# Kernel tuning notes

Hardware: AMD Instinct MI355X
Metric: run time of the kernel (lower is better)

## Reference

```python
import jax, jax.numpy as jnp
import numpy as np

NEG_SLOPE = 0.2
EPS = 1e-16  # PyG softmax denominator epsilon


def _gatv2_layer(x, src, dst, n_nodes, W_l, W_r, att, bias):
    """Single-head GATv2Conv (PyG defaults, self loops already in src/dst).
    x: [N, F_in]; src/dst: [E]; W_l/W_r: [F_in, F_out]; att: [F_out]; bias: [F_out].
    """
    x_l = x @ W_l                       # source transform [N, F_out]
    x_r = x @ W_r                       # target transform [N, F_out]
    # per-edge attention logit: a^T LeakyReLU(x_l[j] + x_r[i])
    e = jax.nn.leaky_relu(x_l[src] + x_r[dst], NEG_SLOPE) @ att  # [E]
    # softmax over incoming edges of each destination node
    e_max = jax.ops.segment_max(e, dst, num_segments=n_nodes)    # [N]
    ex = jnp.exp(e - e_max[dst])                                  # [E]
    denom = jax.ops.segment_sum(ex, dst, num_segments=n_nodes)   # [N]
    alpha = ex / (denom[dst] + EPS)                               # [E]
    out = jax.ops.segment_sum(alpha[:, None] * x_l[src], dst, num_segments=n_nodes)
    return out + bias


def setup_inputs() -> dict:
    key = jax.random.key(0)
    N, E = 50000, 800000
    IN, HID, OUT = 128, 64, 64
    ks = jax.random.split(key, 12)
    x = jax.random.normal(ks[0], (N, IN), dtype=jnp.float32)
    edge_index = jax.random.randint(ks[1], (2, E), 0, N, dtype=jnp.int64)
    s1 = float(1.0 / np.sqrt(IN))
    s2 = float(1.0 / np.sqrt(HID))
    return {
        "x": x,
        "edge_index": edge_index,
        "W1_l": jax.random.uniform(ks[2], (IN, HID), jnp.float32, -s1, s1),
        "W1_r": jax.random.uniform(ks[3], (IN, HID), jnp.float32, -s1, s1),
        "att1": jax.random.uniform(ks[4], (HID,), jnp.float32, -s2, s2),
        "b1": jnp.zeros((HID,), jnp.float32),
        "W2_l": jax.random.uniform(ks[5], (HID, OUT), jnp.float32, -s2, s2),
        "W2_r": jax.random.uniform(ks[6], (HID, OUT), jnp.float32, -s2, s2),
        "att2": jax.random.uniform(ks[7], (OUT,), jnp.float32, -s2, s2),
        "b2": jnp.zeros((OUT,), jnp.float32),
    }


def reference(x, edge_index, W1_l, W1_r, att1, b1, W2_l, W2_r, att2, b2):
    n = x.shape[0]
    loop = jnp.arange(n, dtype=edge_index.dtype)
    src = jnp.concatenate([edge_index[0], loop])  # add self loops (PyG default)
    dst = jnp.concatenate([edge_index[1], loop])
    h = _gatv2_layer(x, src, dst, n, W1_l, W1_r, att1, b1)
    h = jax.nn.relu(h)
    out = _gatv2_layer(h, src, dst, n, W2_l, W2_r, att2, b2)
    return out
```

## Files before the change

### kernel.cpp

```cpp
#include <hip/hip_runtime.h>
#include <math.h>

#define NEG_SLOPE 0.2f
#define EPSV 1e-16f
#define NEG_HUGE -1e30f
#define CAP 64
#define GH 512

typedef short short8 __attribute__((ext_vector_type(8)));
typedef float f32x4 __attribute__((ext_vector_type(4)));
typedef unsigned short u16;


__global__ __launch_bounds__(256) void k_wpack(
        const float* __restrict__ W1l, const float* __restrict__ W1r,
        const float* __restrict__ W2l, const float* __restrict__ W2r,
        u16* __restrict__ w1hi, u16* __restrict__ w1lo,
        u16* __restrict__ w2hi, u16* __restrict__ w2lo,
        int* __restrict__ cnt, int CN) {
    const int idx = blockIdx.x * 256 + threadIdx.x;
    const int G = gridDim.x * 256;
    for (int i = idx; i < CN; i += G) cnt[i] = 0;
    const int T1 = 128 * 128, T2 = 64 * 128;
    if (idx >= T1 + T2) return;
    u16 *dhi, *dlo; const float *Wl, *Wr; int li;
    if (idx < T1) { dhi = w1hi; dlo = w1lo; Wl = W1l; Wr = W1r; li = idx; }
    else          { dhi = w2hi; dlo = w2lo; Wl = W2l; Wr = W2r; li = idx - T1; }
    const int j = li & 7, l = (li >> 3) & 63, t = (li >> 9) & 7, c = li >> 12;
    const int k = c * 32 + (l >> 4) * 8 + j;
    const int n = t * 16 + (l & 15);
    const float v = (n < 64) ? Wl[k * 64 + n] : Wr[k * 64 + (n - 64)];
    const unsigned u = __float_as_uint(v);
    dhi[li] = (u16)(u >> 16);
    const float hif = __uint_as_float(u & 0xffff0000u);
    dlo[li] = (u16)(__float_as_uint(v - hif) >> 16);
}

__device__ __forceinline__ void split8(const float* fs, short8& ahi, short8& alo) {
#pragma unroll
    for (int j = 0; j < 8; ++j) {
        const unsigned u = __float_as_uint(fs[j]);
        ahi[j] = (short)(u >> 16);
        const float hif = __uint_as_float(u & 0xffff0000u);
        alo[j] = (short)(__float_as_uint(fs[j] - hif) >> 16);
    }
}

template <int K>
__device__ __forceinline__ void gemm_mfma_tile(const float* __restrict__ X,
                                               const u16* __restrict__ whi,
                                               const u16* __restrict__ wlo,
                                               float* __restrict__ xl,
                                               float* __restrict__ xr,
                                               int N, int tile) {
    const int lane = threadIdx.x & 63;
    const int w = threadIdx.x >> 6;
    const int rowbase = tile * 64 + w * 16;
    const int m = lane & 15, q = lane >> 4;
    int ar = rowbase + m; if (ar > N - 1) ar = N - 1;
    const float* arow = X + (size_t)ar * K + q * 8;
    f32x4 acc[8];
#pragma unroll
    for (int t = 0; t < 8; ++t) acc[t] = (f32x4){0.f, 0.f, 0.f, 0.f};
#pragma unroll
    for (int c = 0; c < K / 32; ++c) {
        const float4 f0 = *(const float4*)(arow + c * 32);
        const float4 f1 = *(const float4*)(arow + c * 32 + 4);
        const float fs[8] = {f0.x, f0.y, f0.z, f0.w, f1.x, f1.y, f1.z, f1.w};
        short8 ahi, alo;
        split8(fs, ahi, alo);
        const u16* bp = whi + ((size_t)(c * 8) * 64 + lane) * 8;
        const u16* bq = wlo + ((size_t)(c * 8) * 64 + lane) * 8;
#pragma unroll
        for (int t = 0; t < 8; ++t) {
            const short8 bhi = *(const short8*)(bp + t * 64 * 8);
            const short8 blo = *(const short8*)(bq + t * 64 * 8);
            acc[t] = __builtin_amdgcn_mfma_f32_16x16x32_bf16(bhi, ahi, acc[t], 0, 0, 0);
            acc[t] = __builtin_amdgcn_mfma_f32_16x16x32_bf16(blo, ahi, acc[t], 0, 0, 0);
            acc[t] = __builtin_amdgcn_mfma_f32_16x16x32_bf16(bhi, alo, acc[t], 0, 0, 0);
        }
    }
    const int row = rowbase + m;
    if (row < N) {
#pragma unroll
        for (int t = 0; t < 8; ++t) {
            const int colb = t * 16 + q * 4;
            float4 v;
            v.x = acc[t][0]; v.y = acc[t][1]; v.z = acc[t][2]; v.w = acc[t][3];
            float* dstp = (t < 4) ? (xl + (size_t)row * 64 + colb)
                                  : (xr + (size_t)row * 64 + (colb - 64));
            *(float4*)dstp = v;
        }
    }
}

template <int K>
__global__ __launch_bounds__(256) void k_hist_gemm(const int* __restrict__ ei, int E,
                                                   int* __restrict__ cnt,
                                                   u16* __restrict__ csrc,
                                                   const float* __restrict__ X,
                                                   const u16* __restrict__ whi,
                                                   const u16* __restrict__ wlo,
                                                   float* __restrict__ xl,
                                                   float* __restrict__ xr,
                                                   int N, int NP) {
    if ((int)blockIdx.x < GH) {
        const int cls = blockIdx.x & 7;
        const int stripe = blockIdx.x >> 3;
        const int NS = GH >> 3;
        const int tid = threadIdx.x;
        const int* srcp = ei;
        const int* dstp = ei + E;
        int* cntc = cnt + cls * NP;
        if ((E & 3) == 0) {
            for (int base = stripe * 1024; base < E; base += NS * 1024) {
                const int e4 = base + tid * 4;
                if (e4 < E) {
                    const int4 d4 = *(const int4*)(dstp + e4);
                    const int4 s4 = *(const int4*)(srcp + e4);
                    if ((d4.x & 7) == cls) {
                        const int slot = atomicAdd(&cntc[d4.x >> 3], 1);
                        csrc[(size_t)d4.x * CAP + slot] = (u16)s4.x;
                    }
                    if ((d4.y & 7) == cls) {
                        const int slot = atomicAdd(&cntc[d4.y >> 3], 1);
                        csrc[(size_t)d4.y * CAP + slot] = (u16)s4.y;
                    }
                    if ((d4.z & 7) == cls) {
                        const int slot = atomicAdd(&cntc[d4.z >> 3], 1);
                        csrc[(size_t)d4.z * CAP + slot] = (u16)s4.z;
                    }
                    if ((d4.w & 7) == cls) {
                        const int slot = atomicAdd(&cntc[d4.w >> 3], 1);
                        csrc[(size_t)d4.w * CAP + slot] = (u16)s4.w;
                    }
                }
            }
        } else {
            for (int base = stripe * 256; base < E; base += NS * 256) {
                const int e = base + tid;
                if (e < E) {
                    const int d = dstp[e];
                    if ((d & 7) == cls) {
                        const int s = srcp[e];
                        const int slot = atomicAdd(&cntc[d >> 3], 1);
                        csrc[(size_t)d * CAP + slot] = (u16)s;
                    }
                }
            }
        }
        for (int k = tid; ((stripe + k * NS) << 3) + cls < N; k += 256) {
            const int d = ((stripe + k * NS) << 3) + cls;
            const int slot = atomicAdd(&cntc[d >> 3], 1);
            csrc[(size_t)d * CAP + slot] = (u16)d;
        }
    } else {
        gemm_mfma_tile<K>(X, whi, wlo, xl, xr, N, blockIdx.x - GH);
    }
}

template <int K>
__global__ __launch_bounds__(256) void k_gemm(const float* __restrict__ X,
                                              const u16* __restrict__ whi,
                                              const u16* __restrict__ wlo,
                                              float* __restrict__ xl,
                                              float* __restrict__ xr, int N) {
    gemm_mfma_tile<K>(X, whi, wlo, xl, xr, N, blockIdx.x);
}

__global__ __launch_bounds__(256) void k_attn(const float* __restrict__ xl,
                                              const float* xr,
                                              const float* __restrict__ att,
                                              const int* __restrict__ cnt,
                                              const u16* __restrict__ csrc,
                                              const float* __restrict__ bias,
                                              float* out, int N, int NP, int relu) {
    const int lane = threadIdx.x & 63;
    const int g = lane >> 4;
    const int i = lane & 15;
    const int dst = blockIdx.x * 4 + (threadIdx.x >> 6);
    if (dst >= N) return;
    const float4 xrv = *(const float4*)(xr + (size_t)dst * 64 + i * 4);
    const float4 aw  = *(const float4*)(att + i * 4);
    const int deg = cnt[(dst & 7) * NP + (dst >> 3)];
    const int sidx = (int)csrc[(size_t)dst * CAP + ((lane < deg) ? lane : 0)];
    float l = 0.0f;
    float4 acc = {0.0f, 0.0f, 0.0f, 0.0f};
    for (int t = 0; t < deg; t += 16) {
        const int s0 = t + g, s1 = t + 4 + g, s2 = t + 8 + g, s3 = t + 12 + g;
        const bool v0 = s0 < deg, v1 = s1 < deg, v2 = s2 < deg, v3 = s3 < deg;
        const int src0 = __shfl(sidx, s0, 64);
        const int src1 = __shfl(sidx, s1, 64);
        const int src2 = __shfl(sidx, s2, 64);
        const int src3 = __shfl(sidx, s3, 64);
        const float4 va = *(const float4*)(xl + (size_t)src0 * 64 + i * 4);
        const float4 vb = *(const float4*)(xl + (size_t)src1 * 64 + i * 4);
        const float4 vc = *(const float4*)(xl + (size_t)src2 * 64 + i * 4);
        const float4 vd = *(const float4*)(xl + (size_t)src3 * 64 + i * 4);
        float t0, p0, p1, p2, p3;
        t0 = va.x + xrv.x; t0 = fmaxf(t0, NEG_SLOPE * t0); p0 = aw.x * t0;
        t0 = va.y + xrv.y; t0 = fmaxf(t0, NEG_SLOPE * t0); p0 = fmaf(aw.y, t0, p0);
        t0 = va.z + xrv.z; t0 = fmaxf(t0, NEG_SLOPE * t0); p0 = fmaf(aw.z, t0, p0);
        t0 = va.w + xrv.w; t0 = fmaxf(t0, NEG_SLOPE * t0); p0 = fmaf(aw.w, t0, p0);
        t0 = vb.x + xrv.x; t0 = fmaxf(t0, NEG_SLOPE * t0); p1 = aw.x * t0;
        t0 = vb.y + xrv.y; t0 = fmaxf(t0, NEG_SLOPE * t0); p1 = fmaf(aw.y, t0, p1);
        t0 = vb.z + xrv.z; t0 = fmaxf(t0, NEG_SLOPE * t0); p1 = fmaf(aw.z, t0, p1);
        t0 = vb.w + xrv.w; t0 = fmaxf(t0, NEG_SLOPE * t0); p1 = fmaf(aw.w, t0, p1);
        t0 = vc.x + xrv.x; t0 = fmaxf(t0, NEG_SLOPE * t0); p2 = aw.x * t0;
        t0 = vc.y + xrv.y; t0 = fmaxf(t0, NEG_SLOPE * t0); p2 = fmaf(aw.y, t0, p2);
        t0 = vc.z + xrv.z; t0 = fmaxf(t0, NEG_SLOPE * t0); p2 = fmaf(aw.z, t0, p2);
        t0 = vc.w + xrv.w; t0 = fmaxf(t0, NEG_SLOPE * t0); p2 = fmaf(aw.w, t0, p2);
        t0 = vd.x + xrv.x; t0 = fmaxf(t0, NEG_SLOPE * t0); p3 = aw.x * t0;
        t0 = vd.y + xrv.y; t0 = fmaxf(t0, NEG_SLOPE * t0); p3 = fmaf(aw.y, t0, p3);
        t0 = vd.z + xrv.z; t0 = fmaxf(t0, NEG_SLOPE * t0); p3 = fmaf(aw.z, t0, p3);
        t0 = vd.w + xrv.w; t0 = fmaxf(t0, NEG_SLOPE * t0); p3 = fmaf(aw.w, t0, p3);
        p0 += __shfl_xor(p0, 1, 64); p1 += __shfl_xor(p1, 1, 64);
        p2 += __shfl_xor(p2, 1, 64); p3 += __shfl_xor(p3, 1, 64);
        p0 += __shfl_xor(p0, 2, 64); p1 += __shfl_xor(p1, 2, 64);
        p2 += __shfl_xor(p2, 2, 64); p3 += __shfl_xor(p3, 2, 64);
        p0 += __shfl_xor(p0, 4, 64); p1 += __shfl_xor(p1, 4, 64);
        p2 += __shfl_xor(p2, 4, 64); p3 += __shfl_xor(p3, 4, 64);
        p0 += __shfl_xor(p0, 8, 64); p1 += __shfl_xor(p1, 8, 64);
        p2 += __shfl_xor(p2, 8, 64); p3 += __shfl_xor(p3, 8, 64);
        const float d0 = __expf(v0 ? p0 : NEG_HUGE);
        const float d1 = __expf(v1 ? p1 : NEG_HUGE);
        const float d2 = __expf(v2 ? p2 : NEG_HUGE);
        const float d3 = __expf(v3 ? p3 : NEG_HUGE);
        l += (d0 + d1) + (d2 + d3);
        acc.x = fmaf(d0, va.x, fmaf(d1, vb.x, fmaf(d2, vc.x, fmaf(d3, vd.x, acc.x))));
        acc.y = fmaf(d0, va.y, fmaf(d1, vb.y, fmaf(d2, vc.y, fmaf(d3, vd.y, acc.y))));
        acc.z = fmaf(d0, va.z, fmaf(d1, vb.z, fmaf(d2, vc.z, fmaf(d3, vd.z, acc.z))));
        acc.w = fmaf(d0, va.w, fmaf(d1, vb.w, fmaf(d2, vc.w, fmaf(d3, vd.w, acc.w))));
    }
#pragma unroll
    for (int o = 16; o <= 32; o <<= 1) {
        l     += __shfl_xor(l, o, 64);
        acc.x += __shfl_xor(acc.x, o, 64);
        acc.y += __shfl_xor(acc.y, o, 64);
        acc.z += __shfl_xor(acc.z, o, 64);
        acc.w += __shfl_xor(acc.w, o, 64);
    }
    if (g == 0) {
        const float4 bv = *(const float4*)(bias + i * 4);
        const float inv = 1.0f / (l + EPSV);
        float4 r;
        r.x = fmaf(acc.x, inv, bv.x);
        r.y = fmaf(acc.y, inv, bv.y);
        r.z = fmaf(acc.z, inv, bv.z);
        r.w = fmaf(acc.w, inv, bv.w);
        if (relu) {
            r.x = fmaxf(r.x, 0.0f); r.y = fmaxf(r.y, 0.0f);
            r.z = fmaxf(r.z, 0.0f); r.w = fmaxf(r.w, 0.0f);
        }
        *(float4*)(out + (size_t)dst * 64 + i * 4) = r;
    }
}


extern "C" void kernel_launch(void* const* d_in, const int* in_sizes, int n_in,
                              void* d_out, int out_size, void* d_ws, size_t ws_size,
                              hipStream_t stream) {
    const float* x    = (const float*)d_in[0];
    const int*   ei   = (const int*)d_in[1];
    const float* W1l  = (const float*)d_in[2];
    const float* W1r  = (const float*)d_in[3];
    const float* att1 = (const float*)d_in[4];
    const float* b1   = (const float*)d_in[5];
    const float* W2l  = (const float*)d_in[6];
    const float* W2r  = (const float*)d_in[7];
    const float* att2 = (const float*)d_in[8];
    const float* b2   = (const float*)d_in[9];

    const int N  = in_sizes[0] / 128;
    const int E  = in_sizes[1] / 2;
    const int NP = (((N + 7) >> 3) + 31) & ~31;

    int* wsi   = (int*)d_ws;
    int* cnt   = wsi;
    u16* csrc  = (u16*)(cnt + 8 * NP);
    u16* w1hi  = csrc + (size_t)N * CAP;
    u16* w1lo  = w1hi + 16384;
    u16* w2hi  = w1lo + 16384;
    u16* w2lo  = w2hi + 8192;
    float* buf1 = (float*)(w2lo + 8192);
    float* buf2 = buf1 + (size_t)N * 64;
    float* fout = (float*)d_out;

    const dim3 b256(256);
    const int gGemm = (N + 63) / 64;
    const int gAttn = (N + 3) / 4;

    k_wpack<<<(128 * 128 + 64 * 128 + 255) / 256, b256, 0, stream>>>(
        W1l, W1r, W2l, W2r, w1hi, w1lo, w2hi, w2lo, cnt, 8 * NP);

    k_hist_gemm<128><<<GH + gGemm, b256, 0, stream>>>(ei, E, cnt, csrc,
                                                      x, w1hi, w1lo, fout, buf1, N, NP);
    k_attn<<<gAttn, b256, 0, stream>>>(fout, buf1, att1, cnt, csrc, b1, buf2, N, NP, 1);

    k_gemm<64><<<gGemm, b256, 0, stream>>>(buf2, w2hi, w2lo, buf1, fout, N);
    k_attn<<<gAttn, b256, 0, stream>>>(buf1, fout, att2, cnt, csrc, b2, fout, N, NP, 0);
}
```

Measured before the change: 205.7 us.

## Pre-seed self loops in wpack, widen histogram batching, add nontemporal GEMM I/O

Self-loop insertion moves out of the histogram kernel into the weight-pack kernel, which sets each node's count to 1 and writes slot 0 directly, so those atomics disappear. The histogram phase now processes 8 edges per thread and issues all atomics before the scatter stores to expose more memory-level parallelism, and GH is doubled to 1024 histogram blocks. The GEMM tile uses nontemporal loads and stores for X and the outputs. Doubling GH adds blocks that compete with the GEMM blocks, and nontemporal stores of xl/xr may hurt the following attention kernel, which reads them back.

```diff
diff --git a/kernel.cpp b/kernel.cpp
--- a/kernel.cpp
+++ b/kernel.cpp
@@ -5,7 +5,7 @@
 #define EPSV 1e-16f
 #define NEG_HUGE -1e30f
 #define CAP 64
-#define GH 512
+#define GH 1024
 
 typedef short short8 __attribute__((ext_vector_type(8)));
 typedef float f32x4 __attribute__((ext_vector_type(4)));
@@ -17,10 +17,17 @@
         const float* __restrict__ W2l, const float* __restrict__ W2r,
         u16* __restrict__ w1hi, u16* __restrict__ w1lo,
         u16* __restrict__ w2hi, u16* __restrict__ w2lo,
-        int* __restrict__ cnt, int CN) {
+        int* __restrict__ cnt, u16* __restrict__ csrc, int N, int NP) {
     const int idx = blockIdx.x * 256 + threadIdx.x;
     const int G = gridDim.x * 256;
-    for (int i = idx; i < CN; i += G) cnt[i] = 0;
+    const int CN = 8 * NP;
+    for (int i = idx; i < CN; i += G) {
+        const int cls = i / NP;
+        const int r = i - cls * NP;
+        const int d = r * 8 + cls;
+        cnt[i] = (d < N) ? 1 : 0;
+    }
+    for (int d = idx; d < N; d += G) csrc[(size_t)d * CAP] = (u16)d;
     const int T1 = 128 * 128, T2 = 64 * 128;
     if (idx >= T1 + T2) return;
     u16 *dhi, *dlo; const float *Wl, *Wr; int li;
@@ -64,9 +71,9 @@
     for (int t = 0; t < 8; ++t) acc[t] = (f32x4){0.f, 0.f, 0.f, 0.f};
 #pragma unroll
     for (int c = 0; c < K / 32; ++c) {
-        const float4 f0 = *(const float4*)(arow + c * 32);
-        const float4 f1 = *(const float4*)(arow + c * 32 + 4);
-        const float fs[8] = {f0.x, f0.y, f0.z, f0.w, f1.x, f1.y, f1.z, f1.w};
+        const f32x4 f0 = __builtin_nontemporal_load((const f32x4*)(arow + c * 32));
+        const f32x4 f1 = __builtin_nontemporal_load((const f32x4*)(arow + c * 32 + 4));
+        const float fs[8] = {f0[0], f0[1], f0[2], f0[3], f1[0], f1[1], f1[2], f1[3]};
         short8 ahi, alo;
         split8(fs, ahi, alo);
         const u16* bp = whi + ((size_t)(c * 8) * 64 + lane) * 8;
@@ -85,11 +92,9 @@
 #pragma unroll
         for (int t = 0; t < 8; ++t) {
             const int colb = t * 16 + q * 4;
-            float4 v;
-            v.x = acc[t][0]; v.y = acc[t][1]; v.z = acc[t][2]; v.w = acc[t][3];
             float* dstp = (t < 4) ? (xl + (size_t)row * 64 + colb)
                                   : (xr + (size_t)row * 64 + (colb - 64));
-            *(float4*)dstp = v;
+            __builtin_nontemporal_store(acc[t], (f32x4*)dstp);
         }
     }
 }
@@ -112,27 +117,25 @@
         const int* srcp = ei;
         const int* dstp = ei + E;
         int* cntc = cnt + cls * NP;
-        if ((E & 3) == 0) {
-            for (int base = stripe * 1024; base < E; base += NS * 1024) {
-                const int e4 = base + tid * 4;
-                if (e4 < E) {
-                    const int4 d4 = *(const int4*)(dstp + e4);
-                    const int4 s4 = *(const int4*)(srcp + e4);
-                    if ((d4.x & 7) == cls) {
-                        const int slot = atomicAdd(&cntc[d4.x >> 3], 1);
-                        csrc[(size_t)d4.x * CAP + slot] = (u16)s4.x;
+        if ((E & 7) == 0) {
+            for (int base = stripe * 2048; base < E; base += NS * 2048) {
+                const int e8 = base + tid * 8;
+                if (e8 < E) {
+                    const int4 da = *(const int4*)(dstp + e8);
+                    const int4 db = *(const int4*)(dstp + e8 + 4);
+                    const int4 sa = *(const int4*)(srcp + e8);
+                    const int4 sb = *(const int4*)(srcp + e8 + 4);
+                    const int d[8] = {da.x, da.y, da.z, da.w, db.x, db.y, db.z, db.w};
+                    const int s[8] = {sa.x, sa.y, sa.z, sa.w, sb.x, sb.y, sb.z, sb.w};
+                    bool m[8]; int sl[8];
+#pragma unroll
+                    for (int j = 0; j < 8; ++j) {
+                        m[j] = (d[j] & 7) == cls;
+                        if (m[j]) sl[j] = atomicAdd(&cntc[d[j] >> 3], 1);
                     }
-                    if ((d4.y & 7) == cls) {
-                        const int slot = atomicAdd(&cntc[d4.y >> 3], 1);
-                        csrc[(size_t)d4.y * CAP + slot] = (u16)s4.y;
-                    }
-                    if ((d4.z & 7) == cls) {
-                        const int slot = atomicAdd(&cntc[d4.z >> 3], 1);
-                        csrc[(size_t)d4.z * CAP + slot] = (u16)s4.z;
-                    }
-                    if ((d4.w & 7) == cls) {
-                        const int slot = atomicAdd(&cntc[d4.w >> 3], 1);
-                        csrc[(size_t)d4.w * CAP + slot] = (u16)s4.w;
+#pragma unroll
+                    for (int j = 0; j < 8; ++j) {
+                        if (m[j]) csrc[(size_t)d[j] * CAP + sl[j]] = (u16)s[j];
                     }
                 }
             }
@@ -140,19 +143,14 @@
             for (int base = stripe * 256; base < E; base += NS * 256) {
                 const int e = base + tid;
                 if (e < E) {
-                    const int d = dstp[e];
-                    if ((d & 7) == cls) {
-                        const int s = srcp[e];
-                        const int slot = atomicAdd(&cntc[d >> 3], 1);
-                        csrc[(size_t)d * CAP + slot] = (u16)s;
+                    const int dd = dstp[e];
+                    if ((dd & 7) == cls) {
+                        const int ss = srcp[e];
+                        const int slot = atomicAdd(&cntc[dd >> 3], 1);
+                        csrc[(size_t)dd * CAP + slot] = (u16)ss;
                     }
                 }
             }
-        }
-        for (int k = tid; ((stripe + k * NS) << 3) + cls < N; k += 256) {
-            const int d = ((stripe + k * NS) << 3) + cls;
-            const int slot = atomicAdd(&cntc[d >> 3], 1);
-            csrc[(size_t)d * CAP + slot] = (u16)d;
         }
     } else {
         gemm_mfma_tile<K>(X, whi, wlo, xl, xr, N, blockIdx.x - GH);
@@ -291,7 +289,7 @@
     const int gAttn = (N + 3) / 4;
 
     k_wpack<<<(128 * 128 + 64 * 128 + 255) / 256, b256, 0, stream>>>(
-        W1l, W1r, W2l, W2r, w1hi, w1lo, w2hi, w2lo, cnt, 8 * NP);
+        W1l, W1r, W2l, W2r, w1hi, w1lo, w2hi, w2lo, cnt, csrc, N, NP);
 
     k_hist_gemm<128><<<GH + gGemm, b256, 0, stream>>>(ei, E, cnt, csrc,
                                                       x, w1hi, w1lo, fout, buf1, N, NP);
```

After: 228.1 us. 10.9% more time.
